# Kernel optimization log

Hardware: AMD Instinct MI355X
Metric: run time of the kernel (lower is better)

The kernel has to match this reference:

```python
import jax, jax.numpy as jnp
import numpy as np

TOKENS = 16384
INPUT_DIM = 2048
NUM_EXPERTS = 16
K = 2


def setup_inputs() -> dict:
    key = jax.random.key(0)
    kx, kn, kw, kb = jax.random.split(key, 4)
    x = jax.random.normal(kx, (TOKENS, INPUT_DIM), dtype=jnp.float32)
    noise = jax.random.normal(kn, (TOKENS, NUM_EXPERTS), dtype=jnp.float32)
    # nn.Linear params: weight [out, in], bias [out]; kaiming-uniform-ish init
    bound = 1.0 / np.sqrt(INPUT_DIM)
    W = jax.random.uniform(kw, (NUM_EXPERTS, INPUT_DIM), dtype=jnp.float32, minval=-bound, maxval=bound)
    b = jax.random.uniform(kb, (NUM_EXPERTS,), dtype=jnp.float32, minval=-bound, maxval=bound)
    return {"x": x, "noise": noise, "W": W, "b": b}


def reference(x, noise, W, b):
    # logits: [tokens, num_experts]
    logits = jnp.einsum("td,ed->te", x, W) + b
    noisy_logits = logits + noise * 0.1
    top_k_values, top_k_indices = jax.lax.top_k(noisy_logits, K)  # [tokens, K]
    weights = jax.nn.softmax(top_k_values, axis=-1)               # [tokens, K]
    # scatter weights back into dense [tokens, num_experts] (zeros elsewhere)
    one_hot = jax.nn.one_hot(top_k_indices, NUM_EXPERTS, dtype=logits.dtype)  # [tokens, K, E]
    sparse_weights = jnp.einsum("tke,tk->te", one_hot, weights)
    return sparse_weights
```

## Files before the change

kernel.cpp:

```cpp
#include <hip/hip_runtime.h>
#include <hip/hip_bf16.h>
#include <math.h>

#define TOKENS 16384
#define DIM    2048
#define NEXP   16
#define CHUNK  256
#define NCHUNK (DIM / CHUNK)
#define TPB    16
#define NWAVE  4

typedef float fvec4 __attribute__((ext_vector_type(4)));
typedef float f32_as1 __attribute__((address_space(1)));
typedef float f32_as3 __attribute__((address_space(3)));

__device__ __forceinline__ void async_row(const float* gp, float* lp) {
    __builtin_amdgcn_global_load_lds((const f32_as1*)(const void*)gp,
                                     (f32_as3*)(uintptr_t)lp, 16, 0, 0);
}

__global__ __launch_bounds__(256, 2) void gating_moe_kernel(
    const float* __restrict__ x,
    const float* __restrict__ noise,
    const float* __restrict__ W,
    const float* __restrict__ b,
    float* __restrict__ out)
{
    __shared__ __align__(16) float xb[2][TPB][CHUNK];
    __shared__ __align__(16) float wb[2][NEXP][CHUNK];

    const int tid  = threadIdx.x;
    const int lane = tid & 63;
    const int w    = tid >> 6;
    const int block_base = blockIdx.x * TPB;
    const int lane4 = lane * 4;

    float r[64];
#pragma unroll
    for (int v = 0; v < 64; ++v) r[v] = 0.0f;

#pragma unroll
    for (int q = 0; q < 4; ++q) {
        const int row = w * 4 + q;
        async_row(x + (size_t)(block_base + row) * DIM + lane4, &xb[0][row][0]);
        async_row(W + (size_t)row * DIM + lane4, &wb[0][row][0]);
    }
    __syncthreads();

    for (int c = 0; c < NCHUNK; ++c) {
        const int cur = c & 1, nxt = cur ^ 1;
        if (c + 1 < NCHUNK) {
#pragma unroll
            for (int q = 0; q < 4; ++q) {
                const int row = w * 4 + q;
                async_row(x + (size_t)(block_base + row) * DIM + (c + 1) * CHUNK + lane4,
                          &xb[nxt][row][0]);
                async_row(W + (size_t)row * DIM + (c + 1) * CHUNK + lane4,
                          &wb[nxt][row][0]);
            }
        }
        fvec4 xv[4];
#pragma unroll
        for (int t = 0; t < 4; ++t)
            xv[t] = *(const fvec4*)&xb[cur][w * 4 + t][lane4];
#pragma unroll
        for (int e = 0; e < NEXP; ++e) {
            fvec4 wv = *(const fvec4*)&wb[cur][e][lane4];
#pragma unroll
            for (int t = 0; t < 4; ++t) {
                r[t * 16 + e] = fmaf(xv[t].x, wv.x,
                               fmaf(xv[t].y, wv.y,
                               fmaf(xv[t].z, wv.z,
                               fmaf(xv[t].w, wv.w, r[t * 16 + e]))));
            }
        }
        __syncthreads();
    }

#pragma unroll
    for (int s = 0; s < 6; ++s) {
        const int dist = 1 << s;
        const bool bsel = (lane >> s) & 1;
        const int n = 64 >> (s + 1);
#pragma unroll
        for (int i = 0; i < n; ++i) {
            float keep = bsel ? r[2 * i + 1] : r[2 * i];
            float send = bsel ? r[2 * i]     : r[2 * i + 1];
            r[i] = keep + __shfl_xor(send, dist);
        }
    }

    const int e = lane & 15;
    const size_t obase = (size_t)block_base * NEXP + (size_t)w * 64;
    float nz   = noise[obase + lane];
    float bias = b[e];
    float noisy = r[0] + bias + 0.1f * nz;

    float v1 = noisy; int i1 = e;
    float v2 = -INFINITY; int i2 = 999;
#pragma unroll
    for (int s = 0; s < 4; ++s) {
        const int d = 1 << s;
        float ov1 = __shfl_xor(v1, d); int oi1 = __shfl_xor(i1, d);
        float ov2 = __shfl_xor(v2, d); int oi2 = __shfl_xor(i2, d);
        bool awin = (v1 > ov1) || (v1 == ov1 && i1 < oi1);
        float t1v = awin ? v1  : ov1;  int t1i = awin ? i1  : oi1;
        float lv  = awin ? ov1 : v1;   int li  = awin ? oi1 : i1;
        float cv  = awin ? v2  : ov2;  int ci  = awin ? i2  : oi2;
        bool bwin = (cv > lv) || (cv == lv && ci < li);
        v1 = t1v; i1 = t1i;
        v2 = bwin ? cv : lv; i2 = bwin ? ci : li;
    }

    float dd = __expf(v2 - v1);
    float w1 = 1.0f / (1.0f + dd);
    float w2 = dd * w1;

    float o = (e == i1) ? w1 : ((e == i2) ? w2 : 0.0f);
    out[obase + lane] = o;
}

extern "C" void kernel_launch(void* const* d_in, const int* in_sizes, int n_in,
                              void* d_out, int out_size, void* d_ws, size_t ws_size,
                              hipStream_t stream) {
    const float* x     = (const float*)d_in[0];
    const float* noise = (const float*)d_in[1];
    const float* W     = (const float*)d_in[2];
    const float* b     = (const float*)d_in[3];
    float* out = (float*)d_out;

    dim3 grid(TOKENS / TPB);
    dim3 block(NWAVE * 64);
    gating_moe_kernel<<<grid, block, 0, stream>>>(x, noise, W, b, out);
}
```

Measured before the change: 195.3 us.

## Load x rows directly into registers with nontemporal loads, keep only W in LDS

```diff
diff --git a/kernel.cpp b/kernel.cpp
--- a/kernel.cpp
+++ b/kernel.cpp
@@ -19,15 +19,14 @@
                                      (f32_as3*)(uintptr_t)lp, 16, 0, 0);
 }
 
-__global__ __launch_bounds__(256, 2) void gating_moe_kernel(
+__global__ __launch_bounds__(256, 4) void gating_moe_kernel(
     const float* __restrict__ x,
     const float* __restrict__ noise,
     const float* __restrict__ W,
     const float* __restrict__ b,
     float* __restrict__ out)
 {
-    __shared__ __align__(16) float xb[2][TPB][CHUNK];
-    __shared__ __align__(16) float wb[2][NEXP][CHUNK];
+    __shared__ __align__(16) fvec4 wbuf[2][NEXP][CHUNK / 4];
 
     const int tid  = threadIdx.x;
     const int lane = tid & 63;
@@ -39,42 +38,58 @@
 #pragma unroll
     for (int v = 0; v < 64; ++v) r[v] = 0.0f;
 
+    const float* xr0 = x + (size_t)(block_base + w * 4 + 0) * DIM + lane4;
+    const float* xr1 = xr0 + DIM;
+    const float* xr2 = xr1 + DIM;
+    const float* xr3 = xr2 + DIM;
+
 #pragma unroll
     for (int q = 0; q < 4; ++q) {
-        const int row = w * 4 + q;
-        async_row(x + (size_t)(block_base + row) * DIM + lane4, &xb[0][row][0]);
-        async_row(W + (size_t)row * DIM + lane4, &wb[0][row][0]);
+        const int e = w * 4 + q;
+        async_row(W + (size_t)e * DIM + lane4, (float*)&wbuf[0][e][0]);
     }
+    fvec4 xv0 = __builtin_nontemporal_load((const fvec4*)xr0);
+    fvec4 xv1 = __builtin_nontemporal_load((const fvec4*)xr1);
+    fvec4 xv2 = __builtin_nontemporal_load((const fvec4*)xr2);
+    fvec4 xv3 = __builtin_nontemporal_load((const fvec4*)xr3);
     __syncthreads();
 
+#pragma unroll
     for (int c = 0; c < NCHUNK; ++c) {
         const int cur = c & 1, nxt = cur ^ 1;
+        fvec4 xn0, xn1, xn2, xn3;
         if (c + 1 < NCHUNK) {
 #pragma unroll
             for (int q = 0; q < 4; ++q) {
-                const int row = w * 4 + q;
-                async_row(x + (size_t)(block_base + row) * DIM + (c + 1) * CHUNK + lane4,
-                          &xb[nxt][row][0]);
-                async_row(W + (size_t)row * DIM + (c + 1) * CHUNK + lane4,
-                          &wb[nxt][row][0]);
+                const int e = w * 4 + q;
+                async_row(W + (size_t)e * DIM + (c + 1) * CHUNK + lane4,
+                          (float*)&wbuf[nxt][e][0]);
             }
+            const int off = (c + 1) * CHUNK;
+            xn0 = __builtin_nontemporal_load((const fvec4*)(xr0 + off));
+            xn1 = __builtin_nontemporal_load((const fvec4*)(xr1 + off));
+            xn2 = __builtin_nontemporal_load((const fvec4*)(xr2 + off));
+            xn3 = __builtin_nontemporal_load((const fvec4*)(xr3 + off));
         }
-        fvec4 xv[4];
+
 #pragma unroll
-        for (int t = 0; t < 4; ++t)
-            xv[t] = *(const fvec4*)&xb[cur][w * 4 + t][lane4];
-#pragma unroll
-        for (int e = 0; e < NEXP; ++e) {
-            fvec4 wv = *(const fvec4*)&wb[cur][e][lane4];
-#pragma unroll
-            for (int t = 0; t < 4; ++t) {
-                r[t * 16 + e] = fmaf(xv[t].x, wv.x,
-                               fmaf(xv[t].y, wv.y,
-                               fmaf(xv[t].z, wv.z,
-                               fmaf(xv[t].w, wv.w, r[t * 16 + e]))));
-            }
+        for (int eb = 0; eb < NEXP; eb += 2) {
+            fvec4 wa = wbuf[cur][eb + 0][lane];
+            fvec4 wc = wbuf[cur][eb + 1][lane];
+#define FMA4(acc, xv, wv) acc = fmaf((xv).x,(wv).x, fmaf((xv).y,(wv).y, \
+                                fmaf((xv).z,(wv).z, fmaf((xv).w,(wv).w,(acc)))))
+            FMA4(r[0  * 16 + eb],     xv0, wa);
+            FMA4(r[1  * 16 + eb],     xv1, wa);
+            FMA4(r[2  * 16 + eb],     xv2, wa);
+            FMA4(r[3  * 16 + eb],     xv3, wa);
+            FMA4(r[0  * 16 + eb + 1], xv0, wc);
+            FMA4(r[1  * 16 + eb + 1], xv1, wc);
+            FMA4(r[2  * 16 + eb + 1], xv2, wc);
+            FMA4(r[3  * 16 + eb + 1], xv3, wc);
+#undef FMA4
         }
         __syncthreads();
+        if (c + 1 < NCHUNK) { xv0 = xn0; xv1 = xn1; xv2 = xn2; xv3 = xn3; }
     }
 
 #pragma unroll
@@ -92,9 +107,8 @@
 
     const int e = lane & 15;
     const size_t obase = (size_t)block_base * NEXP + (size_t)w * 64;
-    float nz   = noise[obase + lane];
-    float bias = b[e];
-    float noisy = r[0] + bias + 0.1f * nz;
+    float nz    = noise[obase + lane];
+    float noisy = r[0] + b[e] + 0.1f * nz;
 
     float v1 = noisy; int i1 = e;
     float v2 = -INFINITY; int i2 = 999;
```

Result: faster. 188.4 us (-3.5%).
